# Kernel tuning notes

Measured on AMD Instinct MI355X. Metric: run time of the kernel, lower is better.

The kernel has to match this reference:

```python
import jax, jax.numpy as jnp
import numpy as np
from jax import lax

B, T, D = 2, 2048, 2048
H, DK, DV = 16, 128, 128
K = 4  # conv kernel size
KEY_DIM = H * DK      # 2048
VAL_DIM = H * DV      # 2048
CONV_DIM = 2 * KEY_DIM + VAL_DIM  # 6144
EPS = 1e-6


def setup_inputs() -> dict:
    key = jax.random.key(0)
    ks = jax.random.split(key, 10)
    s = lambda fan: 1.0 / np.sqrt(fan)
    return {
        "hidden_states": jax.random.normal(ks[0], (B, T, D), jnp.float32),
        "W_qkv": jax.random.normal(ks[1], (D, CONV_DIM), jnp.float32) * s(D),
        "conv_w": jax.random.normal(ks[2], (CONV_DIM, 1, K), jnp.float32) * s(K),
        "W_z": jax.random.normal(ks[3], (D, VAL_DIM), jnp.float32) * s(D),
        "W_b": jax.random.normal(ks[4], (D, H), jnp.float32) * s(D),
        "W_a": jax.random.normal(ks[5], (D, H), jnp.float32) * s(D),
        "dt_bias": jnp.ones((H,), jnp.float32),
        "A_log": jnp.log(jax.random.uniform(ks[6], (H,), jnp.float32, 1e-3, 16.0)),
        "norm_weight": jnp.ones((DV,), jnp.float32),
        "W_out": jax.random.normal(ks[7], (VAL_DIM, D), jnp.float32) * s(VAL_DIM),
    }


def _l2norm(x):
    return x * lax.rsqrt(jnp.sum(x * x, axis=-1, keepdims=True) + 1e-6)


def _gated_delta_rule(q, k, v, g, beta):
    """q,k: [B,T,H,DK]; v: [B,T,H,DV]; g,beta: [B,T,H]. Returns o: [B,T,H,DV]."""
    # time-major for scan
    qT, kT, vT = (jnp.moveaxis(x, 1, 0) for x in (q, k, v))  # [T,B,H,d]
    gT = jnp.moveaxis(g, 1, 0)      # [T,B,H]
    bT = jnp.moveaxis(beta, 1, 0)   # [T,B,H]

    def step(S, inp):
        q_t, k_t, v_t, g_t, b_t = inp
        S = S * jnp.exp(g_t)[..., None, None]                      # decay [B,H,DK,DV]
        kv_mem = jnp.einsum("bhk,bhkv->bhv", k_t, S)               # S^T k
        delta = (v_t - kv_mem) * b_t[..., None]                     # beta-scaled error
        S = S + jnp.einsum("bhk,bhv->bhkv", k_t, delta)
        o_t = jnp.einsum("bhk,bhkv->bhv", q_t, S)
        return S, o_t

    S0 = jnp.zeros((q.shape[0], H, DK, DV), q.dtype)
    _, oT = lax.scan(step, S0, (qT, kT, vT, gT, bT))
    return jnp.moveaxis(oT, 0, 1)  # [B,T,H,DV]


def reference(hidden_states, W_qkv, conv_w, W_z, W_b, W_a, dt_bias, A_log,
              norm_weight, W_out):
    Bs, Ts, _ = hidden_states.shape

    # qkv projection + depthwise causal conv1d + silu
    mixed = hidden_states @ W_qkv                      # [B,T,CONV_DIM]
    xc = jnp.moveaxis(mixed, 1, 2)                     # [B,C,T]
    xc = lax.conv_general_dilated(xc, conv_w, (1,), [(K - 1, 0)],
                                  feature_group_count=CONV_DIM)
    mixed = jax.nn.silu(jnp.moveaxis(xc, 1, 2))        # [B,T,C]

    q, k, v = jnp.split(mixed, [KEY_DIM, 2 * KEY_DIM], axis=-1)
    q = _l2norm(q.reshape(Bs, Ts, H, DK)) * (DK ** -0.5)
    k = _l2norm(k.reshape(Bs, Ts, H, DK))
    v = v.reshape(Bs, Ts, H, DV)

    beta = jax.nn.sigmoid(hidden_states @ W_b)                     # [B,T,H]
    g = -jnp.exp(A_log) * jax.nn.softplus(hidden_states @ W_a + dt_bias)

    o = _gated_delta_rule(q, k, v, g, beta)            # [B,T,H,DV]

    # gated RMSNorm (Mamba2-style: gate first, then normalize)
    z = (hidden_states @ W_z).reshape(Bs, Ts, H, DV)
    o = o * jax.nn.silu(z)
    var = jnp.mean(o * o, axis=-1, keepdims=True)
    o = o * lax.rsqrt(var + EPS) * norm_weight

    return o.reshape(Bs, Ts, VAL_DIM) @ W_out          # [B,T,D]
```

## Files before the change

kernel.cpp:

```cpp
#include <hip/hip_runtime.h>

#define B_ 2
#define T_ 2048
#define D_ 2048
#define H_ 16
#define CONV_DIM_ 6144
#define NC_ 32
#define CK_ 64

typedef __bf16 bf16;
typedef bf16 bf16x8 __attribute__((ext_vector_type(8)));
typedef bf16 bf16x4 __attribute__((ext_vector_type(4)));
typedef float floatx4 __attribute__((ext_vector_type(4)));

__device__ __forceinline__ void async_copy16(bf16* lds, const bf16* g) {
    auto* g1 = (const __attribute__((address_space(1))) unsigned int*)g;
    auto* l3 = (__attribute__((address_space(3))) unsigned int*)lds;
    __builtin_amdgcn_global_load_lds(g1, l3, 16, 0, 0);
}

__global__ void cvt_bf16_kernel(const float* __restrict__ in, bf16* __restrict__ out, int n4) {
    int i = blockIdx.x * 256 + threadIdx.x;
    if (i < n4) {
        float4 v = ((const float4*)in)[i];
        bf16x4 o = { (bf16)v.x, (bf16)v.y, (bf16)v.z, (bf16)v.w };
        *(bf16x4*)(out + 4 * (size_t)i) = o;
    }
}

__global__ void transpose_kernel(const float* __restrict__ in, bf16* __restrict__ out, int R, int Cn) {
    __shared__ float tile[32][33];
    const int c0 = blockIdx.x << 5, r0 = blockIdx.y << 5;
    const int tx = threadIdx.x & 31, ty = threadIdx.x >> 5;
#pragma unroll
    for (int i = 0; i < 4; ++i) {
        int r = ty + (i << 3);
        tile[r][tx] = in[(size_t)(r0 + r) * Cn + c0 + tx];
    }
    __syncthreads();
#pragma unroll
    for (int i = 0; i < 4; ++i) {
        int cc = ty + (i << 3);
        out[(size_t)(c0 + cc) * R + r0 + tx] = (bf16)tile[tx][cc];
    }
}

__global__ void wba_cvt_kernel(const float* __restrict__ Wb, const float* __restrict__ Wa,
                               bf16* __restrict__ Wba) {
    int idx = blockIdx.x * 256 + threadIdx.x;
    int d = idx >> 4, h = idx & 15;
    Wba[(size_t)h * 2048 + d]        = (bf16)Wb[idx];
    Wba[(size_t)(h + 16) * 2048 + d] = (bf16)Wa[idx];
}

template <typename OutT>
__global__ __launch_bounds__(256) void gemm_kernel(
    const bf16* __restrict__ A, const bf16* __restrict__ Bt, OutT* __restrict__ C,
    int M, int N, int K) {
    __shared__ bf16 As[128 * 64];
    __shared__ bf16 Bs[128 * 64];
    const int tid = threadIdx.x;
    const int m0 = blockIdx.y << 7;
    const int n0 = blockIdx.x << 7;
    const int wave = tid >> 6, lane = tid & 63;
    const int wm = (wave >> 1) << 6, wn = (wave & 1) << 6;
    const int lrow = lane & 15, quad = lane >> 4;
    const int rl = lane >> 3;
    const int c8s = (lane & 7) ^ (rl & 7);

    floatx4 acc[4][4];
#pragma unroll
    for (int mt = 0; mt < 4; ++mt)
#pragma unroll
        for (int nt = 0; nt < 4; ++nt)
            acc[mt][nt] = floatx4{0.f, 0.f, 0.f, 0.f};

    for (int k0 = 0; k0 < K; k0 += 64) {
        __syncthreads();
#pragma unroll
        for (int i = 0; i < 4; ++i) {
            const int slot = wave * 4 + i;
            const int r = slot * 8 + rl;
            async_copy16(&As[slot * 512], A + (size_t)(m0 + r) * K + k0 + c8s * 8);
            async_copy16(&Bs[slot * 512], Bt + (size_t)(n0 + r) * K + k0 + c8s * 8);
        }
        __syncthreads();
#pragma unroll
        for (int kk = 0; kk < 64; kk += 32) {
            const int sw = (((kk >> 3) + quad) ^ (lrow & 7)) << 3;
            bf16x8 af[4], bfr[4];
#pragma unroll
            for (int mt = 0; mt < 4; ++mt) {
                af[mt]  = *(const bf16x8*)(&As[((wm + (mt << 4) + lrow) << 6) + sw]);
                bfr[mt] = *(const bf16x8*)(&Bs[((wn + (mt << 4) + lrow) << 6) + sw]);
            }
#pragma unroll
            for (int mt = 0; mt < 4; ++mt)
#pragma unroll
                for (int nt = 0; nt < 4; ++nt)
                    acc[mt][nt] = __builtin_amdgcn_mfma_f32_16x16x32_bf16(af[mt], bfr[nt], acc[mt][nt], 0, 0, 0);
        }
    }
#pragma unroll
    for (int mt = 0; mt < 4; ++mt)
#pragma unroll
        for (int nt = 0; nt < 4; ++nt) {
            const int col = n0 + wn + (nt << 4) + lrow;
            const int rowb = m0 + wm + (mt << 4) + (quad << 2);
#pragma unroll
            for (int i2 = 0; i2 < 4; ++i2)
                C[(size_t)(rowb + i2) * N + col] = (OutT)acc[mt][nt][i2];
        }
}

__global__ __launch_bounds__(512, 2) void gemm256_kernel(
    const bf16* __restrict__ A, const bf16* __restrict__ Bt,
    bf16* __restrict__ C0, bf16* __restrict__ C1,
    int M, int Ncat, int K, int split, int ld0, int ld1) {
    __shared__ bf16 As[2][256 * 64];
    __shared__ bf16 Bs[2][256 * 64];
    const int tid = threadIdx.x;
    const int wave = tid >> 6, lane = tid & 63;
    const int quad = lane >> 4, lrow = lane & 15;
    const int wm = (wave >> 2) << 7;
    const int wn = (wave & 3) << 6;
    const int m0 = blockIdx.y << 8, n0 = blockIdx.x << 8;

    const int srow = tid >> 3;
    const int cu_src = (tid & 7) ^ (srow & 7);
    const bf16* ga[4];
    const bf16* gb[4];
#pragma unroll
    for (int i = 0; i < 4; ++i) {
        ga[i] = A  + (size_t)(m0 + i * 64 + srow) * K + cu_src * 8;
        gb[i] = Bt + (size_t)(n0 + i * 64 + srow) * K + cu_src * 8;
    }

    floatx4 acc[8][4];
#pragma unroll
    for (int mt = 0; mt < 8; ++mt)
#pragma unroll
        for (int nt = 0; nt < 4; ++nt)
            acc[mt][nt] = floatx4{0.f, 0.f, 0.f, 0.f};

    const int KT = K >> 6;
    auto stage = [&](int b, int kt) {
        const int k0 = kt << 6;
#pragma unroll
        for (int i = 0; i < 4; ++i) {
            async_copy16(&As[b][i * 4096 + wave * 512], ga[i] + k0);
            async_copy16(&Bs[b][i * 4096 + wave * 512], gb[i] + k0);
        }
    };
    stage(0, 0);
    stage(1, 1);

    for (int kt = 0; kt < KT; ++kt) {
        if (kt + 1 < KT) asm volatile("s_waitcnt vmcnt(8)" ::: "memory");
        else             asm volatile("s_waitcnt vmcnt(0)" ::: "memory");
        __builtin_amdgcn_sched_barrier(0);
        __builtin_amdgcn_s_barrier();
        __builtin_amdgcn_sched_barrier(0);
        const bf16* as = &As[kt & 1][0];
        const bf16* bs = &Bs[kt & 1][0];
#pragma unroll
        for (int kk = 0; kk < 2; ++kk) {
            const int sw = (((kk << 2) + quad) ^ (lrow & 7)) << 3;
            bf16x8 bfr[4];
#pragma unroll
            for (int nt = 0; nt < 4; ++nt)
                bfr[nt] = *(const bf16x8*)(bs + ((wn + nt * 16 + lrow) << 6) + sw);
#pragma unroll
            for (int mh = 0; mh < 2; ++mh) {
                bf16x8 af[4];
#pragma unroll
                for (int mt = 0; mt < 4; ++mt)
                    af[mt] = *(const bf16x8*)(as + ((wm + (mh * 4 + mt) * 16 + lrow) << 6) + sw);
                __builtin_amdgcn_s_setprio(1);
#pragma unroll
                for (int mt = 0; mt < 4; ++mt)
#pragma unroll
                    for (int nt = 0; nt < 4; ++nt)
                        acc[mh * 4 + mt][nt] = __builtin_amdgcn_mfma_f32_16x16x32_bf16(
                            af[mt], bfr[nt], acc[mh * 4 + mt][nt], 0, 0, 0);
                __builtin_amdgcn_s_setprio(0);
            }
        }
        __builtin_amdgcn_sched_barrier(0);
        __builtin_amdgcn_s_barrier();
        __builtin_amdgcn_sched_barrier(0);
        if (kt + 2 < KT) stage(kt & 1, kt + 2);
    }

    const bool second = (n0 >= split);
    bf16* Cp = second ? C1 : C0;
    const int ldc = second ? ld1 : ld0;
    const int nc0 = second ? n0 - split : n0;
#pragma unroll
    for (int mt = 0; mt < 8; ++mt)
#pragma unroll
        for (int nt = 0; nt < 4; ++nt) {
            const int col = nc0 + wn + nt * 16 + lrow;
            const int rowb = m0 + wm + mt * 16 + (quad << 2);
#pragma unroll
            for (int i2 = 0; i2 < 4; ++i2)
                Cp[(size_t)(rowb + i2) * ldc + col] = (bf16)acc[mt][nt][i2];
        }
}

__global__ void conv_silu_kernel(const bf16* __restrict__ mixed, const float* __restrict__ cw,
                                 bf16* __restrict__ qb, bf16* __restrict__ kb, bf16* __restrict__ vb) {
    const int s = blockIdx.x;
    const int bt = blockIdx.y;
    const int t = bt & (T_ - 1);
    const int b = bt >> 11;
    const int c = (s << 7) + threadIdx.x;
    const size_t base = (size_t)bt * CONV_DIM_ + c;
    const float w0 = cw[c * 4], w1 = cw[c * 4 + 1], w2 = cw[c * 4 + 2], w3 = cw[c * 4 + 3];
    float acc = (float)mixed[base] * w3;
    if (t >= 1) acc += (float)mixed[base - CONV_DIM_] * w2;
    if (t >= 2) acc += (float)mixed[base - 2 * CONV_DIM_] * w1;
    if (t >= 3) acc += (float)mixed[base - 3 * CONV_DIM_] * w0;
    const float val = acc / (1.f + __expf(-acc));

    __shared__ float red[2];
    if (s < 32) {
        float ss = val * val;
#pragma unroll
        for (int o = 1; o < 64; o <<= 1) ss += __shfl_xor(ss, o);
        if ((threadIdx.x & 63) == 0) red[threadIdx.x >> 6] = ss;
        __syncthreads();
        const float scale = rsqrtf(red[0] + red[1] + 1e-6f);
        const int h = s & 15;
        const size_t oidx = (((size_t)(b * H_ + h)) * T_ + t) * 128 + threadIdx.x;
        if (s < 16) qb[oidx] = (bf16)(val * scale * 0.08838834764831845f);
        else        kb[oidx] = (bf16)(val * scale);
    } else {
        const int h = s - 32;
        const size_t oidx = (((size_t)(b * H_ + h)) * T_ + t) * 128 + threadIdx.x;
        vb[oidx] = (bf16)val;
    }
}

__global__ __launch_bounds__(256) void gbeta_mfma_kernel(
    const bf16* __restrict__ Xb, const bf16* __restrict__ Wba,
    const float* __restrict__ dtb, const float* __restrict__ Alog,
    float* __restrict__ gbuf, float* __restrict__ bbuf) {
    const int tid = threadIdx.x, wave = tid >> 6, lane = tid & 63;
    const int ln = lane & 15, qd = lane >> 4;
    const int m0 = blockIdx.x * 64 + wave * 16;
    floatx4 acc0 = {0.f, 0.f, 0.f, 0.f}, acc1 = {0.f, 0.f, 0.f, 0.f};
    const bf16* arow = Xb + (size_t)(m0 + ln) * 2048 + qd * 8;
    const bf16* b0 = Wba + (size_t)ln * 2048 + qd * 8;
    const bf16* b1 = Wba + (size_t)(16 + ln) * 2048 + qd * 8;
    for (int k = 0; k < 2048; k += 32) {
        bf16x8 af  = *(const bf16x8*)(arow + k);
        bf16x8 bf0 = *(const bf16x8*)(b0 + k);
        bf16x8 bf1 = *(const bf16x8*)(b1 + k);
        acc0 = __builtin_amdgcn_mfma_f32_16x16x32_bf16(af, bf0, acc0, 0, 0, 0);
        acc1 = __builtin_amdgcn_mfma_f32_16x16x32_bf16(af, bf1, acc1, 0, 0, 0);
    }
    const float dtbv = dtb[ln], al = __expf(Alog[ln]);
#pragma unroll
    for (int ii = 0; ii < 4; ++ii) {
        const int row = m0 + qd * 4 + ii;
        const int t = row & (T_ - 1), b = row >> 11;
        const size_t o = ((size_t)(b * H_ + ln)) * T_ + t;
        bbuf[o] = 1.f / (1.f + __expf(-acc0[ii]));
        const float xx = acc1[ii] + dtbv;
        const float sp = (xx > 15.f) ? xx : log1pf(__expf(xx));
        gbuf[o] = -al * sp;
    }
}

__global__ __launch_bounds__(256) void qkkt_kernel(const bf16* __restrict__ qb, const bf16* __restrict__ kb,
                                                   float* __restrict__ Araw, float* __restrict__ Mraw) {
    const int u = blockIdx.x;
    const int bh = u >> 5, nc = u & 31;
    const int t0 = nc * CK_;
    const int tid = threadIdx.x, wave = tid >> 6, lane = tid & 63;
    const int qd = lane >> 4, ln = lane & 15;
    __shared__ bf16 Kc[64 * 136], Qc[64 * 136];
    const size_t kbase = ((size_t)bh * T_ + t0) * 128;
#pragma unroll
    for (int it = 0; it < 4; ++it) {
        int idx = it * 256 + tid;
        int row = idx >> 4, c8 = idx & 15;
        *(uint4*)(&Kc[row * 136 + c8 * 8]) = *(const uint4*)(kb + kbase + row * 128 + c8 * 8);
        *(uint4*)(&Qc[row * 136 + c8 * 8]) = *(const uint4*)(qb + kbase + row * 128 + c8 * 8);
    }
    __syncthreads();
#pragma unroll
    for (int nt = 0; nt < 4; ++nt) {
        floatx4 accA = {0.f, 0.f, 0.f, 0.f}, accM = {0.f, 0.f, 0.f, 0.f};
#pragma unroll
        for (int kk = 0; kk < 4; ++kk) {
            bf16x8 bfr = *(const bf16x8*)(&Kc[(nt * 16 + ln) * 136 + kk * 32 + qd * 8]);
            bf16x8 afK = *(const bf16x8*)(&Kc[(wave * 16 + ln) * 136 + kk * 32 + qd * 8]);
            bf16x8 afQ = *(const bf16x8*)(&Qc[(wave * 16 + ln) * 136 + kk * 32 + qd * 8]);
            accA = __builtin_amdgcn_mfma_f32_16x16x32_bf16(afK, bfr, accA, 0, 0, 0);
            accM = __builtin_amdgcn_mfma_f32_16x16x32_bf16(afQ, bfr, accM, 0, 0, 0);
        }
#pragma unroll
        for (int ii = 0; ii < 4; ++ii) {
            int i = wave * 16 + qd * 4 + ii, j = nt * 16 + ln;
            Araw[(size_t)u * 4096 + i * 64 + j] = accA[ii];
            Mraw[(size_t)u * 4096 + i * 64 + j] = accM[ii];
        }
    }
}

__global__ __launch_bounds__(64) void prep_kernel(
    const float* __restrict__ gbuf, const float* __restrict__ bbuf,
    const float* __restrict__ Araw, const float* __restrict__ Mraw,
    float* __restrict__ lamg, float* __restrict__ ratiog,
    bf16* __restrict__ Tg, bf16* __restrict__ Mg) {
    const int u = blockIdx.x, bh = u >> 5, nc = u & 31, t0 = nc * CK_;
    const int lane = threadIdx.x;
    __shared__ float L[64 * 65];
    __shared__ float cv[64], bv[64];
    float g = gbuf[(size_t)bh * T_ + t0 + lane];
    float beta = bbuf[(size_t)bh * T_ + t0 + lane];
    float c = g;
#pragma unroll
    for (int off = 1; off < 64; off <<= 1) {
        float tval = __shfl_up(c, off);
        if (lane >= off) c += tval;
    }
    float c63 = __shfl(c, 63);
    lamg[(size_t)u * 64 + lane] = __expf(c);
    ratiog[(size_t)u * 64 + lane] = __expf(c63 - c);
    cv[lane] = c; bv[lane] = beta;
    __syncthreads();
    for (int i = 0; i < 64; ++i) {
        float a = Araw[(size_t)u * 4096 + i * 64 + lane];
        L[i * 65 + lane] = (lane < i) ? bv[i] * __expf(cv[i] - c) * a : 0.f;
    }
    __syncthreads();
    float t[64];
#pragma unroll
    for (int i = 0; i < 64; ++i) t[i] = (i == lane) ? 1.f : 0.f;
#pragma unroll
    for (int j = 0; j < 63; ++j) {
#pragma unroll
        for (int i = j + 1; i < 64; ++i)
            t[i] -= L[i * 65 + j] * t[j];
    }
#pragma unroll
    for (int i = 0; i < 64; ++i)
        Tg[(size_t)u * 4096 + i * 64 + lane] = (bf16)t[i];
    for (int i = 0; i < 64; ++i) {
        float m = Mraw[(size_t)u * 4096 + i * 64 + lane];
        float mij = (lane <= i) ? __expf(cv[i] - c) * m : 0.f;
        Mg[(size_t)u * 4096 + i * 64 + lane] = (bf16)mij;
    }
}

struct Pref {
    uint4 t2[2], m2[2];
    bf16x8 kf[4], qf[4];
    bf16x8 ktf[2][2];
    float rrv[4], vv[4], lam[4], bet[4], lamlast;
};

__device__ __forceinline__ void load_pref(
    Pref& p, int u, int t0, size_t kbase, int tid, int wave, int ln, int qd,
    int bh, int vbase,
    const bf16* __restrict__ qb, const bf16* __restrict__ kb, const bf16* __restrict__ vb,
    const bf16* __restrict__ Tg, const bf16* __restrict__ Mg,
    const float* __restrict__ lamg, const float* __restrict__ ratiog,
    const float* __restrict__ bbuf) {
#pragma unroll
    for (int it = 0; it < 2; ++it) {
        int idx = it * 256 + tid;
        int row = idx >> 3, c8 = idx & 7;
        p.t2[it] = *(const uint4*)(Tg + (size_t)u * 4096 + row * 64 + c8 * 8);
        p.m2[it] = *(const uint4*)(Mg + (size_t)u * 4096 + row * 64 + c8 * 8);
    }
    const size_t rowoff = kbase + (size_t)(wave * 16 + ln) * 128;
#pragma unroll
    for (int kk = 0; kk < 4; ++kk) {
        p.kf[kk] = *(const bf16x8*)(kb + rowoff + kk * 32 + qd * 8);
        p.qf[kk] = *(const bf16x8*)(qb + rowoff + kk * 32 + qd * 8);
    }
#pragma unroll
    for (int mt = 0; mt < 2; ++mt) {
        const int kd = (wave * 2 + mt) * 16 + ln;
#pragma unroll
        for (int kk2 = 0; kk2 < 2; ++kk2) {
            const int ib = kk2 * 32 + qd * 8;
#pragma unroll
            for (int j = 0; j < 8; ++j)
                p.ktf[mt][kk2][j] = kb[kbase + (size_t)(ib + j) * 128 + kd];
        }
    }
    const int i0 = wave * 16 + qd * 4;
#pragma unroll
    for (int ii = 0; ii < 4; ++ii) {
        p.vv[ii]  = (float)vb[kbase + (size_t)(i0 + ii) * 128 + vbase + ln];
        p.lam[ii] = lamg[(size_t)u * 64 + i0 + ii];
        p.bet[ii] = bbuf[(size_t)bh * T_ + t0 + i0 + ii];
        p.rrv[ii] = ratiog[(size_t)u * 64 + i0 + ii];
    }
    p.lamlast = lamg[(size_t)u * 64 + 63];
}

__global__ __launch_bounds__(256) void seq_kernel(
    const bf16* __restrict__ qb, const bf16* __restrict__ kb, const bf16* __restrict__ vb,
    const bf16* __restrict__ Tg, const bf16* __restrict__ Mg,
    const float* __restrict__ lamg, const float* __restrict__ ratiog,
    const float* __restrict__ bbuf, float* __restrict__ ob) {
    const int bh = blockIdx.x & 31;
    const int vs = blockIdx.x >> 5;
    const int vbase = vs * 16;
    const int tid = threadIdx.x;
    const int wave = tid >> 6, lane = tid & 63;
    const int qd = lane >> 4, ln = lane & 15;

    __shared__ bf16 Tt[64 * 72], Mm[64 * 72];
    __shared__ bf16 bT[16 * 72], Dt[16 * 72], Dtr[16 * 72];
    __shared__ bf16 Sbf[16 * 136];
    __shared__ float Sf[16 * 132];

    for (int idx = tid; idx < 16 * 132; idx += 256) Sf[idx] = 0.f;
    for (int idx = tid; idx < 16 * 136; idx += 256) Sbf[idx] = (bf16)0.f;

    Pref cur, nxt;
    load_pref(cur, bh * NC_, 0, (size_t)bh * T_ * 128, tid, wave, ln, qd, bh, vbase,
              qb, kb, vb, Tg, Mg, lamg, ratiog, bbuf);
    __syncthreads();

    for (int nc = 0; nc < NC_; ++nc) {
        const int t0 = nc * CK_;
        const size_t kbase = ((size_t)bh * T_ + t0) * 128;

#pragma unroll
        for (int it = 0; it < 2; ++it) {
            int idx = it * 256 + tid;
            int row = idx >> 3, c8 = idx & 7;
            *(uint4*)(&Tt[row * 72 + c8 * 8]) = cur.t2[it];
            *(uint4*)(&Mm[row * 72 + c8 * 8]) = cur.m2[it];
        }

        {
            const int ncn = (nc + 1 < NC_) ? nc + 1 : nc;
            load_pref(nxt, bh * NC_ + ncn, ncn * CK_, ((size_t)bh * T_ + (size_t)ncn * CK_) * 128,
                      tid, wave, ln, qd, bh, vbase, qb, kb, vb, Tg, Mg, lamg, ratiog, bbuf);
        }

        floatx4 ks = {0.f, 0.f, 0.f, 0.f};
#pragma unroll
        for (int kk = 0; kk < 4; ++kk) {
            bf16x8 bf = *(const bf16x8*)(&Sbf[ln * 136 + kk * 32 + qd * 8]);
            ks = __builtin_amdgcn_mfma_f32_16x16x32_bf16(cur.kf[kk], bf, ks, 0, 0, 0);
        }
        {
            const int i0 = wave * 16 + qd * 4;
            bf16x4 bw;
#pragma unroll
            for (int ii = 0; ii < 4; ++ii)
                bw[ii] = (bf16)(cur.bet[ii] * (cur.vv[ii] - cur.lam[ii] * ks[ii]));
            *(bf16x4*)(&bT[ln * 72 + i0]) = bw;
        }
        __syncthreads();

        {
            floatx4 acc = {0.f, 0.f, 0.f, 0.f};
#pragma unroll
            for (int kk = 0; kk < 2; ++kk) {
                bf16x8 af = *(const bf16x8*)(&Tt[(wave * 16 + ln) * 72 + kk * 32 + qd * 8]);
                bf16x8 bf = *(const bf16x8*)(&bT[ln * 72 + kk * 32 + qd * 8]);
                acc = __builtin_amdgcn_mfma_f32_16x16x32_bf16(af, bf, acc, 0, 0, 0);
            }
            const int i0 = wave * 16 + qd * 4;
            bf16x4 dw = { (bf16)acc[0], (bf16)acc[1], (bf16)acc[2], (bf16)acc[3] };
            *(bf16x4*)(&Dt[ln * 72 + i0]) = dw;
            bf16x4 dwr = { (bf16)(acc[0] * cur.rrv[0]), (bf16)(acc[1] * cur.rrv[1]),
                           (bf16)(acc[2] * cur.rrv[2]), (bf16)(acc[3] * cur.rrv[3]) };
            *(bf16x4*)(&Dtr[ln * 72 + i0]) = dwr;
        }
        __syncthreads();

        {
            floatx4 acc = {0.f, 0.f, 0.f, 0.f};
#pragma unroll
            for (int kk = 0; kk < 4; ++kk) {
                bf16x8 bf = *(const bf16x8*)(&Sbf[ln * 136 + kk * 32 + qd * 8]);
                acc = __builtin_amdgcn_mfma_f32_16x16x32_bf16(cur.qf[kk], bf, acc, 0, 0, 0);
            }
            floatx4 o;
#pragma unroll
            for (int ii = 0; ii < 4; ++ii) o[ii] = acc[ii] * cur.lam[ii];
#pragma unroll
            for (int kk = 0; kk < 2; ++kk) {
                bf16x8 af = *(const bf16x8*)(&Mm[(wave * 16 + ln) * 72 + kk * 32 + qd * 8]);
                bf16x8 bf = *(const bf16x8*)(&Dt[ln * 72 + kk * 32 + qd * 8]);
                o = __builtin_amdgcn_mfma_f32_16x16x32_bf16(af, bf, o, 0, 0, 0);
            }
            const int i0 = wave * 16 + qd * 4;
#pragma unroll
            for (int ii = 0; ii < 4; ++ii)
                ob[kbase + (size_t)(i0 + ii) * 128 + vbase + ln] = o[ii];
        }
#pragma unroll
        for (int mt = 0; mt < 2; ++mt) {
            const int kt = wave * 2 + mt;
            floatx4 acc = {0.f, 0.f, 0.f, 0.f};
#pragma unroll
            for (int kk = 0; kk < 2; ++kk) {
                bf16x8 bf = *(const bf16x8*)(&Dtr[ln * 72 + kk * 32 + qd * 8]);
                acc = __builtin_amdgcn_mfma_f32_16x16x32_bf16(cur.ktf[mt][kk], bf, acc, 0, 0, 0);
            }
            const int k0 = kt * 16 + qd * 4;
            floatx4 sold = *(floatx4*)(&Sf[ln * 132 + k0]);
#pragma unroll
            for (int ii = 0; ii < 4; ++ii) sold[ii] = sold[ii] * cur.lamlast + acc[ii];
            *(floatx4*)(&Sf[ln * 132 + k0]) = sold;
        }
        __syncthreads();
        {
            const int vloc = tid >> 4, k0 = (tid & 15) * 8;
            floatx4 s0 = *(floatx4*)(&Sf[vloc * 132 + k0]);
            floatx4 s1 = *(floatx4*)(&Sf[vloc * 132 + k0 + 4]);
            bf16x8 sb = { (bf16)s0[0], (bf16)s0[1], (bf16)s0[2], (bf16)s0[3],
                          (bf16)s1[0], (bf16)s1[1], (bf16)s1[2], (bf16)s1[3] };
            *(bf16x8*)(&Sbf[vloc * 136 + k0]) = sb;
        }
        __syncthreads();
        cur = nxt;
    }
}

__global__ void gated_norm_kernel(const float* __restrict__ ob, const bf16* __restrict__ z,
                                  const float* __restrict__ nw, bf16* __restrict__ onorm) {
    const int idx = blockIdx.x;
    const int h = idx & (H_ - 1);
    const int bt = idx >> 4;
    const int t = bt & (T_ - 1);
    const int b = bt >> 11;
    const int tid = threadIdx.x;
    const size_t obase = (((size_t)(b * H_ + h)) * T_ + t) * 128;
    const size_t zbase = (size_t)bt * 2048 + (h << 7);
    float o1 = ob[obase + tid], o2 = ob[obase + tid + 64];
    const float z1 = (float)z[zbase + tid], z2 = (float)z[zbase + tid + 64];
    o1 *= z1 / (1.f + __expf(-z1));
    o2 *= z2 / (1.f + __expf(-z2));
    float ss = o1 * o1 + o2 * o2;
#pragma unroll
    for (int o = 1; o < 64; o <<= 1) ss += __shfl_xor(ss, o);
    const float scale = rsqrtf(ss * (1.f / 128.f) + 1e-6f);
    onorm[zbase + tid]      = (bf16)(o1 * scale * nw[tid]);
    onorm[zbase + tid + 64] = (bf16)(o2 * scale * nw[tid + 64]);
}

extern "C" void kernel_launch(void* const* d_in, const int* in_sizes, int n_in,
                              void* d_out, int out_size, void* d_ws, size_t ws_size,
                              hipStream_t stream) {
    const float* X    = (const float*)d_in[0];
    const float* Wqkv = (const float*)d_in[1];
    const float* cw   = (const float*)d_in[2];
    const float* Wz   = (const float*)d_in[3];
    const float* Wb   = (const float*)d_in[4];
    const float* Wa   = (const float*)d_in[5];
    const float* dtb  = (const float*)d_in[6];
    const float* Alog = (const float*)d_in[7];
    const float* nw   = (const float*)d_in[8];
    const float* Wout = (const float*)d_in[9];
    float* out = (float*)d_out;

    char* ws = (char*)d_ws;
    size_t off = 0;
    auto alloc = [&](size_t bytes) -> char* {
        char* p = ws + off;
        off += (bytes + 255) & ~(size_t)255;
        return p;
    };
    bf16*  Xb      = (bf16*)alloc((size_t)B_ * T_ * D_ * 2);
    char*  wcat_p  = alloc((size_t)8192 * 2048 * 2);
    bf16*  Wcat    = (bf16*)wcat_p;
    bf16*  Woutt   = (bf16*)alloc((size_t)D_ * D_ * 2);
    bf16*  Wba     = (bf16*)alloc((size_t)32 * 2048 * 2);
    char*  mixed_p = alloc((size_t)B_ * T_ * CONV_DIM_ * 2);
    bf16*  mixedb  = (bf16*)mixed_p;
    bf16*  zb      = (bf16*)alloc((size_t)B_ * T_ * D_ * 2);
    bf16*  kbuf    = (bf16*)alloc((size_t)B_ * T_ * D_ * 2);
    bf16*  vbuf    = (bf16*)alloc((size_t)B_ * T_ * D_ * 2);
    float* gbuf    = (float*)alloc((size_t)B_ * T_ * H_ * 4);
    float* bbuf    = (float*)alloc((size_t)B_ * T_ * H_ * 4);
    float* Mraw    = (float*)alloc((size_t)1024 * 4096 * 4);
    bf16*  Tg      = (bf16*)alloc((size_t)1024 * 4096 * 2);
    bf16*  Mg      = (bf16*)alloc((size_t)1024 * 4096 * 2);
    float* lamg    = (float*)alloc((size_t)1024 * 64 * 4);
    float* ratiog  = (float*)alloc((size_t)1024 * 64 * 4);
    bf16*  qbuf    = (bf16*)wcat_p;
    float* obuf    = (float*)mixed_p;
    float* Araw    = (float*)(mixed_p + (size_t)B_ * T_ * D_ * 4);
    bf16*  onorm   = (bf16*)Xb;

    cvt_bf16_kernel<<<dim3((B_ * T_ * D_ / 4 + 255) / 256), dim3(256), 0, stream>>>(X, Xb, B_ * T_ * D_ / 4);
    transpose_kernel<<<dim3(CONV_DIM_ / 32, D_ / 32), dim3(256), 0, stream>>>(Wqkv, Wcat, D_, CONV_DIM_);
    transpose_kernel<<<dim3(D_ / 32, D_ / 32), dim3(256), 0, stream>>>(Wz, Wcat + (size_t)CONV_DIM_ * D_, D_, D_);
    transpose_kernel<<<dim3(D_ / 32, D_ / 32), dim3(256), 0, stream>>>(Wout, Woutt, D_, D_);
    wba_cvt_kernel<<<dim3(128), dim3(256), 0, stream>>>(Wb, Wa, Wba);

    gemm256_kernel<<<dim3(8192 / 256, B_ * T_ / 256), dim3(512), 0, stream>>>(
        Xb, Wcat, mixedb, zb, B_ * T_, 8192, D_, CONV_DIM_, CONV_DIM_, D_);

    gbeta_mfma_kernel<<<dim3(64), dim3(256), 0, stream>>>(Xb, Wba, dtb, Alog, gbuf, bbuf);
    conv_silu_kernel<<<dim3(CONV_DIM_ / 128, B_ * T_), dim3(128), 0, stream>>>(mixedb, cw, qbuf, kbuf, vbuf);

    qkkt_kernel<<<dim3(1024), dim3(256), 0, stream>>>(qbuf, kbuf, Araw, Mraw);
    prep_kernel<<<dim3(1024), dim3(64), 0, stream>>>(gbuf, bbuf, Araw, Mraw, lamg, ratiog, Tg, Mg);
    seq_kernel<<<dim3(256), dim3(256), 0, stream>>>(qbuf, kbuf, vbuf, Tg, Mg, lamg, ratiog, bbuf, obuf);

    gated_norm_kernel<<<dim3(B_ * T_ * H_), dim3(64), 0, stream>>>(obuf, zb, nw, onorm);

    gemm_kernel<float><<<dim3(D_ / 128, B_ * T_ / 128), dim3(256), 0, stream>>>(
        onorm, Woutt, out, B_ * T_, D_, D_);
}
```

Before: 645.1 us.

## Restructure gemm256 into 4-stage BK=32 pipeline with interleaved half-tile MFMA phases

Rewrites the 256x256 GEMM main loop from a double-buffered BK=64 scheme to a four-buffer BK=32 ring with three tiles in flight. Each iteration is split into two phases: the upper and lower halves of the M rows. The next tile's A and B async copies are issued between these phases, so LDS fills overlap MFMA work. A new swizzled LDS layout packs two 32-wide rows per 64-element line to avoid bank conflicts. This hides global-load latency better, at the cost of more barriers per K-step and tighter vmcnt bookkeeping.

```diff
diff --git a/kernel.cpp b/kernel.cpp
--- a/kernel.cpp
+++ b/kernel.cpp
@@ -117,8 +117,8 @@
     const bf16* __restrict__ A, const bf16* __restrict__ Bt,
     bf16* __restrict__ C0, bf16* __restrict__ C1,
     int M, int Ncat, int K, int split, int ld0, int ld1) {
-    __shared__ bf16 As[2][256 * 64];
-    __shared__ bf16 Bs[2][256 * 64];
+    __shared__ bf16 As[4][256 * 32];
+    __shared__ bf16 Bs[4][256 * 32];
     const int tid = threadIdx.x;
     const int wave = tid >> 6, lane = tid & 63;
     const int quad = lane >> 4, lrow = lane & 15;
@@ -126,15 +126,21 @@
     const int wn = (wave & 3) << 6;
     const int m0 = blockIdx.y << 8, n0 = blockIdx.x << 8;
 
-    const int srow = tid >> 3;
-    const int cu_src = (tid & 7) ^ (srow & 7);
-    const bf16* ga[4];
-    const bf16* gb[4];
-#pragma unroll
-    for (int i = 0; i < 4; ++i) {
-        ga[i] = A  + (size_t)(m0 + i * 64 + srow) * K + cu_src * 8;
-        gb[i] = Bt + (size_t)(n0 + i * 64 + srow) * K + cu_src * 8;
-    }
+    const bf16* gA[2];
+    const bf16* gB[2];
+#pragma unroll
+    for (int i = 0; i < 2; ++i) {
+        const int q = wave * 2 + i;
+        const int u = (lane & 7) ^ (lane >> 3);
+        const int row = (q * 8 + (lane >> 3)) * 2 + (u >> 2);
+        const int col = (u & 3) * 8;
+        gA[i] = A  + (size_t)(m0 + row) * K + col;
+        gB[i] = Bt + (size_t)(n0 + row) * K + col;
+    }
+
+    auto loff = [](int row, int qd) -> int {
+        return ((row >> 1) << 6) + (((((row & 1) << 2) | qd) ^ ((row >> 1) & 7)) << 3);
+    };
 
     floatx4 acc[8][4];
 #pragma unroll
@@ -143,53 +149,70 @@
         for (int nt = 0; nt < 4; ++nt)
             acc[mt][nt] = floatx4{0.f, 0.f, 0.f, 0.f};
 
-    const int KT = K >> 6;
-    auto stage = [&](int b, int kt) {
-        const int k0 = kt << 6;
-#pragma unroll
-        for (int i = 0; i < 4; ++i) {
-            async_copy16(&As[b][i * 4096 + wave * 512], ga[i] + k0);
-            async_copy16(&Bs[b][i * 4096 + wave * 512], gb[i] + k0);
-        }
-    };
-    stage(0, 0);
-    stage(1, 1);
-
-    for (int kt = 0; kt < KT; ++kt) {
-        if (kt + 1 < KT) asm volatile("s_waitcnt vmcnt(8)" ::: "memory");
-        else             asm volatile("s_waitcnt vmcnt(0)" ::: "memory");
+    const int KT = K >> 5;
+
+#pragma unroll
+    for (int t = 0; t < 3; ++t) {
+        async_copy16(&As[t][(wave * 2 + 0) * 512], gA[0] + t * 32);
+        async_copy16(&As[t][(wave * 2 + 1) * 512], gA[1] + t * 32);
+        async_copy16(&Bs[t][(wave * 2 + 0) * 512], gB[0] + t * 32);
+        async_copy16(&Bs[t][(wave * 2 + 1) * 512], gB[1] + t * 32);
+    }
+    asm volatile("s_waitcnt vmcnt(8)" ::: "memory");
+    __builtin_amdgcn_s_barrier();
+
+    for (int t = 0; t < KT; ++t) {
+        const int b = t & 3;
+        const bf16* as = &As[b][0];
+        const bf16* bs = &Bs[b][0];
+        bf16x8 bfr[4], af[4];
+#pragma unroll
+        for (int nt = 0; nt < 4; ++nt)
+            bfr[nt] = *(const bf16x8*)(bs + loff(wn + nt * 16 + lrow, quad));
+#pragma unroll
+        for (int mt = 0; mt < 4; ++mt)
+            af[mt] = *(const bf16x8*)(as + loff(wm + mt * 16 + lrow, quad));
+        if (t + 2 < KT)       asm volatile("s_waitcnt vmcnt(4)" ::: "memory");
+        else if (t + 2 == KT) asm volatile("s_waitcnt vmcnt(0)" ::: "memory");
+        if (t + 3 < KT) {
+            const int bn = (t + 3) & 3;
+            async_copy16(&As[bn][(wave * 2 + 0) * 512], gA[0] + (t + 3) * 32);
+            async_copy16(&As[bn][(wave * 2 + 1) * 512], gA[1] + (t + 3) * 32);
+        }
+        __builtin_amdgcn_s_barrier();
+        asm volatile("s_waitcnt lgkmcnt(0)" ::: "memory");
+        __builtin_amdgcn_sched_barrier(0);
+        __builtin_amdgcn_s_setprio(1);
+#pragma unroll
+        for (int mt = 0; mt < 4; ++mt)
+#pragma unroll
+            for (int nt = 0; nt < 4; ++nt)
+                acc[mt][nt] = __builtin_amdgcn_mfma_f32_16x16x32_bf16(
+                    af[mt], bfr[nt], acc[mt][nt], 0, 0, 0);
+        __builtin_amdgcn_s_setprio(0);
         __builtin_amdgcn_sched_barrier(0);
         __builtin_amdgcn_s_barrier();
+#pragma unroll
+        for (int mt = 0; mt < 4; ++mt)
+            af[mt] = *(const bf16x8*)(as + loff(wm + 64 + mt * 16 + lrow, quad));
+        if (t + 3 < KT) {
+            const int bn = (t + 3) & 3;
+            async_copy16(&Bs[bn][(wave * 2 + 0) * 512], gB[0] + (t + 3) * 32);
+            async_copy16(&Bs[bn][(wave * 2 + 1) * 512], gB[1] + (t + 3) * 32);
+        }
+        __builtin_amdgcn_s_barrier();
+        asm volatile("s_waitcnt lgkmcnt(0)" ::: "memory");
         __builtin_amdgcn_sched_barrier(0);
-        const bf16* as = &As[kt & 1][0];
-        const bf16* bs = &Bs[kt & 1][0];
-#pragma unroll
-        for (int kk = 0; kk < 2; ++kk) {
-            const int sw = (((kk << 2) + quad) ^ (lrow & 7)) << 3;
-            bf16x8 bfr[4];
+        __builtin_amdgcn_s_setprio(1);
+#pragma unroll
+        for (int mt = 0; mt < 4; ++mt)
 #pragma unroll
             for (int nt = 0; nt < 4; ++nt)
-                bfr[nt] = *(const bf16x8*)(bs + ((wn + nt * 16 + lrow) << 6) + sw);
-#pragma unroll
-            for (int mh = 0; mh < 2; ++mh) {
-                bf16x8 af[4];
-#pragma unroll
-                for (int mt = 0; mt < 4; ++mt)
-                    af[mt] = *(const bf16x8*)(as + ((wm + (mh * 4 + mt) * 16 + lrow) << 6) + sw);
-                __builtin_amdgcn_s_setprio(1);
-#pragma unroll
-                for (int mt = 0; mt < 4; ++mt)
-#pragma unroll
-                    for (int nt = 0; nt < 4; ++nt)
-                        acc[mh * 4 + mt][nt] = __builtin_amdgcn_mfma_f32_16x16x32_bf16(
-                            af[mt], bfr[nt], acc[mh * 4 + mt][nt], 0, 0, 0);
-                __builtin_amdgcn_s_setprio(0);
-            }
-        }
+                acc[4 + mt][nt] = __builtin_amdgcn_mfma_f32_16x16x32_bf16(
+                    af[mt], bfr[nt], acc[4 + mt][nt], 0, 0, 0);
+        __builtin_amdgcn_s_setprio(0);
         __builtin_amdgcn_sched_barrier(0);
         __builtin_amdgcn_s_barrier();
-        __builtin_amdgcn_sched_barrier(0);
-        if (kt + 2 < KT) stage(kt & 1, kt + 2);
     }
 
     const bool second = (n0 >= split);
```

Result: no change. 643.1 us (-0.3%).
